# Optimization experiments

Measured on AMD Instinct MI355X. Metric: run time of the kernel, lower is better.

Reference implementation:

```python
import jax, jax.numpy as jnp
import numpy as np

B, T_IN, H, V, MAXLEN = 128, 256, 512, 32, 128


def gru_cell(x, h, Wih, Whh, bih, bhh):
    # torch GRU cell: gates ordered (r, z, n)
    gi = x @ Wih.T + bih            # [B, 3H]
    gh = h @ Whh.T + bhh            # [B, 3H]
    ir, iz, inn = jnp.split(gi, 3, axis=-1)
    hr, hz, hn = jnp.split(gh, 3, axis=-1)
    r = jax.nn.sigmoid(ir + hr)
    z = jax.nn.sigmoid(iz + hz)
    n = jnp.tanh(inn + r * hn)
    return (1.0 - z) * n + z * h


def run_gru_layer(xs, Wih, Whh, bih, bhh):
    # xs: [B, T, D] -> outputs [B, T, H], final hidden [B, H]
    h0 = jnp.zeros((xs.shape[0], Whh.shape[1]), xs.dtype)

    def step(h, x):
        hn = gru_cell(x, h, Wih, Whh, bih, bhh)
        return hn, hn

    hT, ys = jax.lax.scan(step, h0, jnp.swapaxes(xs, 0, 1))
    return jnp.swapaxes(ys, 0, 1), hT


def setup_inputs() -> dict:
    key = jax.random.key(0)
    ks = jax.random.split(key, 24)
    s = 1.0 / np.sqrt(H)

    def p(k, shape):
        return (jax.random.normal(k, shape, jnp.float32) * s).astype(jnp.float32)

    return {
        "x": jax.random.normal(ks[0], (B, T_IN, 2), jnp.float32),
        "emb": p(ks[1], (V, H)),
        # encoder GRU: layer0 input dim 2, layer1 input dim H
        "enc_Wih0": p(ks[2], (3 * H, 2)), "enc_Whh0": p(ks[3], (3 * H, H)),
        "enc_bih0": p(ks[4], (3 * H,)), "enc_bhh0": p(ks[5], (3 * H,)),
        "enc_Wih1": p(ks[6], (3 * H, H)), "enc_Whh1": p(ks[7], (3 * H, H)),
        "enc_bih1": p(ks[8], (3 * H,)), "enc_bhh1": p(ks[9], (3 * H,)),
        # decoder GRU: layer0 input dim 2H (embedded+context), layer1 input dim H
        "dec_Wih0": p(ks[10], (3 * H, 2 * H)), "dec_Whh0": p(ks[11], (3 * H, H)),
        "dec_bih0": p(ks[12], (3 * H,)), "dec_bhh0": p(ks[13], (3 * H,)),
        "dec_Wih1": p(ks[14], (3 * H, H)), "dec_Whh1": p(ks[15], (3 * H, H)),
        "dec_bih1": p(ks[16], (3 * H,)), "dec_bhh1": p(ks[17], (3 * H,)),
        "q_W": p(ks[18], (H, H)), "q_b": p(ks[19], (H,)),
        "out_W": p(ks[20], (V, H)), "out_b": p(ks[21], (V,)),
    }


def reference(x, emb,
              enc_Wih0, enc_Whh0, enc_bih0, enc_bhh0,
              enc_Wih1, enc_Whh1, enc_bih1, enc_bhh1,
              dec_Wih0, dec_Whh0, dec_bih0, dec_bhh0,
              dec_Wih1, dec_Whh1, dec_bih1, dec_bhh1,
              q_W, q_b, out_W, out_b):
    # ----- encoder: 2-layer GRU over trajectory points -----
    y0, h0 = run_gru_layer(x, enc_Wih0, enc_Whh0, enc_bih0, enc_bhh0)
    enc_outs, h1 = run_gru_layer(y0, enc_Wih1, enc_Whh1, enc_bih1, enc_bhh1)
    hidden0 = jnp.stack([h0, h1])                      # [L, B, H]
    bsz = x.shape[0]

    def step(carry, _):
        hidden, tok = carry                            # [L,B,H], [B] int
        embedded = emb[tok]                            # [B, H]
        query = hidden[-1] @ q_W.T + q_b               # [B, H]
        scores = jnp.einsum('bh,bth->bt', query, enc_outs)
        attn_w = jax.nn.softmax(scores, axis=-1)       # [B, T_in]
        context = jnp.einsum('bt,bth->bh', attn_w, enc_outs)
        rnn_in = jnp.concatenate([embedded, context], axis=-1)  # [B, 2H]
        g0 = gru_cell(rnn_in, hidden[0], dec_Wih0, dec_Whh0, dec_bih0, dec_bhh0)
        g1 = gru_cell(g0, hidden[1], dec_Wih1, dec_Whh1, dec_bih1, dec_bhh1)
        logits = g1 @ out_W.T + out_b                  # [B, V]
        tok_next = jnp.argmax(logits, axis=-1)
        return (jnp.stack([g0, g1]), tok_next), (logits, attn_w)

    tok0 = jnp.zeros((bsz,), jnp.int32)
    (hidden_f, _), (logits_seq, attn_seq) = jax.lax.scan(
        step, (hidden0, tok0), None, length=MAXLEN)
    vec_out = jnp.swapaxes(logits_seq, 0, 1)           # [B, max_len, V]
    attn = jnp.swapaxes(attn_seq, 0, 1)                # [B, max_len, T_in]
    return vec_out, hidden_f, attn
```

## Files before the change

kernel.cpp:

```cpp
#include <hip/hip_runtime.h>
#include <math.h>

#define BB 128
#define TT 256
#define HH 512
#define VV 32
#define MLEN 128
#define SLOT 65536

#define WT_OFF 0
#define QT_OFF 24576
#define PR_OFF 26624
#define SC_OFF 28416
#define SM_FLOATS 32512

typedef long long ll;

struct P {
    const float *x, *emb;
    const float *eWih0, *eWhh0, *ebih0, *ebhh0;
    const float *eWih1, *eWhh1, *ebih1, *ebhh1;
    const float *dWih0, *dWhh0, *dbih0, *dbhh0;
    const float *dWih1, *dWhh1, *dbih1, *dbhh1;
    const float *qW, *qb, *outW, *outb;
    float *ws;
    float *vecO, *hidO, *attnO;
};

__device__ __forceinline__ float sigf(float v) { return 1.0f / (1.0f + __expf(-v)); }

__device__ __forceinline__ float ldA(const float* p) {
    return __hip_atomic_load(p, __ATOMIC_RELAXED, __HIP_MEMORY_SCOPE_AGENT);
}
__device__ __forceinline__ void stA(float* p, float v) {
    __hip_atomic_store(p, v, __ATOMIC_RELAXED, __HIP_MEMORY_SCOPE_AGENT);
}
__device__ __forceinline__ int ldAi(const int* p) {
    return __hip_atomic_load(p, __ATOMIC_RELAXED, __HIP_MEMORY_SCOPE_AGENT);
}
__device__ __forceinline__ void stAi(int* p, int v) {
    __hip_atomic_store(p, v, __ATOMIC_RELAXED, __HIP_MEMORY_SCOPE_AGENT);
}

__device__ __forceinline__ void gbar(int* W, int target) {
    __syncthreads();
    if (threadIdx.x == 0) {
        int par = target & 1;
        int g = blockIdx.x & 15;
        int* gc = W + 32 + (par * 16 + g) * 32;
        if (__hip_atomic_fetch_add(gc, 1, __ATOMIC_RELAXED, __HIP_MEMORY_SCOPE_AGENT) == 15) {
            __hip_atomic_store(gc, 0, __ATOMIC_RELAXED, __HIP_MEMORY_SCOPE_AGENT);
            int* rc = W + 1056 + par * 32;
            if (__hip_atomic_fetch_add(rc, 1, __ATOMIC_RELAXED, __HIP_MEMORY_SCOPE_AGENT) == 15) {
                __hip_atomic_store(rc, 0, __ATOMIC_RELAXED, __HIP_MEMORY_SCOPE_AGENT);
                __hip_atomic_store(W, target, __ATOMIC_RELAXED, __HIP_MEMORY_SCOPE_AGENT);
            }
        }
        while (__hip_atomic_load(W, __ATOMIC_RELAXED, __HIP_MEMORY_SCOPE_AGENT) < target)
            __builtin_amdgcn_s_sleep(2);
    }
    __syncthreads();
}

__global__ __launch_bounds__(512, 1) void kmain(P p) {
    __shared__ __align__(16) float smu[SM_FLOATS];
    const int tid = threadIdx.x;
    const int lane = tid & 63;
    const int wv = tid >> 6;
    const int blk = blockIdx.x;

    int* W = (int*)p.ws;
    int* tok = W + 4096;
    float* f = (float*)p.ws + 8192;
    float* eh0 = f;
    float* eh1 = f + 2 * SLOT;
    float* inp = f + 4 * SLOT;
    float* qbm = f + 5 * SLOT;
    float* scoresB = f + 6 * SLOT;
    float* T = f + 6 * SLOT + SLOT / 2;
    float* xT = T + 3 * HH * VV;
    float* encO = f + (SLOT / 4) * 33;

    const float4* t4 = (const float4*)smu;
    const float4* t4q = (const float4*)(smu + QT_OFF);

    const int jg = blk >> 1;
    const int bh = blk & 1;
    const int b2 = bh * 64 + lane;
    int bar = 0;

    {
        stA(eh0 + blk * 1024 + tid, 0.0f);
        stA(eh0 + blk * 1024 + 512 + tid, 0.0f);
        if (tid < 256) {
            int idx = blk * 256 + tid;
            int t = idx >> 8, c = (idx >> 7) & 1, b = idx & 127;
            stA(xT + idx, p.x[((ll)b * TT + t) * 2 + c]);
        }
        if (tid < 192) {
            int unit = blk * 192 + tid;
            int v = unit & 31, gj = unit >> 5;
            const float* wrow = p.dWih0 + (ll)gj * 1024;
            const float* erow = p.emb + (ll)v * HH;
            float acc = 0.0f;
#pragma unroll 8
            for (int d = 0; d < HH; ++d) acc = fmaf(wrow[d], erow[d], acc);
            stA(T + unit, acc);
        }
#pragma unroll
        for (int jl = 0; jl < 4; ++jl)
            smu[QT_OFF + jl * 512 + tid] = p.qW[((ll)(jg * 4 + jl)) * HH + tid];
#pragma unroll
        for (int r = 0; r < 24; ++r) {
            int g = r >> 2, jl = r & 3, j = jg * 4 + jl;
            const float* src = (g < 3) ? (p.eWhh0 + (ll)(g * HH + j) * HH)
                                       : (p.eWih1 + (ll)((g - 3) * HH + j) * HH);
            smu[WT_OFF + r * 512 + tid] = src[tid];
        }
#pragma unroll
        for (int r = 0; r < 12; ++r) {
            int g = r >> 2, jl = r & 3, j = jg * 4 + jl;
            smu[WT_OFF + (24 + r) * 512 + tid] = p.eWhh1[(ll)(g * HH + j) * HH + tid];
        }
        gbar(W, ++bar);
    }

    for (int t = 0; t <= TT; ++t) {
        const float* h0s = eh0 + (((t + 1) & 1) ? SLOT : 0);
        float*       h0d = eh0 + ((t & 1) ? SLOT : 0);
        const float* h1s = eh1 + (((t + 1) & 1) ? SLOT : 0);
        float*       h1d = eh1 + ((t & 1) ? SLOT : 0);

        smu[PR_OFF + tid] = 0.0f;
        smu[PR_OFF + 512 + tid] = 0.0f;
        smu[PR_OFF + 1024 + tid] = 0.0f;
        if (tid < 256) smu[PR_OFF + 1536 + tid] = 0.0f;
        __syncthreads();

        {
            const int ds0 = wv * 64;
            float acc[36];
#pragma unroll
            for (int r = 0; r < 36; ++r) acc[r] = 0.0f;
            float av[2][8], bv[2][8];
#pragma unroll
            for (int u = 0; u < 8; ++u) av[0][u] = ldA(h0s + (ll)(ds0 + u) * BB + b2);
#pragma unroll
            for (int u = 0; u < 8; ++u) bv[0][u] = ldA(h1s + (ll)(ds0 + u) * BB + b2);
#pragma unroll
            for (int c = 0; c < 8; ++c) {
                const int cb = c & 1, pb = cb ^ 1;
                if (c < 7) {
                    const int dn = ds0 + (c + 1) * 8;
#pragma unroll
                    for (int u = 0; u < 8; ++u) av[pb][u] = ldA(h0s + (ll)(dn + u) * BB + b2);
#pragma unroll
                    for (int u = 0; u < 8; ++u) bv[pb][u] = ldA(h1s + (ll)(dn + u) * BB + b2);
                }
                const int db = ds0 + c * 8;
#pragma unroll
                for (int h2 = 0; h2 < 2; ++h2) {
                    const int q4 = (db + h2 * 4) >> 2;
#pragma unroll
                    for (int r = 0; r < 24; ++r) {
                        float4 w = t4[r * 128 + q4];
                        acc[r] = fmaf(w.x, av[cb][h2 * 4 + 0], acc[r]);
                        acc[r] = fmaf(w.y, av[cb][h2 * 4 + 1], acc[r]);
                        acc[r] = fmaf(w.z, av[cb][h2 * 4 + 2], acc[r]);
                        acc[r] = fmaf(w.w, av[cb][h2 * 4 + 3], acc[r]);
                    }
#pragma unroll
                    for (int r = 0; r < 12; ++r) {
                        float4 w = t4[(24 + r) * 128 + q4];
                        acc[24 + r] = fmaf(w.x, bv[cb][h2 * 4 + 0], acc[24 + r]);
                        acc[24 + r] = fmaf(w.y, bv[cb][h2 * 4 + 1], acc[24 + r]);
                        acc[24 + r] = fmaf(w.z, bv[cb][h2 * 4 + 2], acc[24 + r]);
                        acc[24 + r] = fmaf(w.w, bv[cb][h2 * 4 + 3], acc[24 + r]);
                    }
                }
            }
#pragma unroll
            for (int r = 0; r < 24; ++r)
                unsafeAtomicAdd(&smu[PR_OFF + r * 64 + lane], acc[r]);
#pragma unroll
            for (int r = 0; r < 12; ++r) {
                int g = r >> 2;
                int prow = (g < 2) ? (12 + g * 4) : 24;
                unsafeAtomicAdd(&smu[PR_OFF + (prow + (r & 3)) * 64 + lane], acc[24 + r]);
            }
        }
        __syncthreads();

        if (wv < 4) {
            if (t < TT) {
                int jl = wv, j = jg * 4 + jl;
                float* pr = smu + PR_OFF;
                float hr = pr[(0 + jl) * 64 + lane] + p.ebhh0[j];
                float hz = pr[(4 + jl) * 64 + lane] + p.ebhh0[HH + j];
                float hn = pr[(8 + jl) * 64 + lane] + p.ebhh0[2 * HH + j];
                float x0 = xT[t * 256 + b2], x1 = xT[t * 256 + 128 + b2];
                float ir = fmaf(p.eWih0[j * 2], x0, fmaf(p.eWih0[j * 2 + 1], x1, p.ebih0[j]));
                float iz = fmaf(p.eWih0[(HH + j) * 2], x0, fmaf(p.eWih0[(HH + j) * 2 + 1], x1, p.ebih0[HH + j]));
                float in_ = fmaf(p.eWih0[(2 * HH + j) * 2], x0, fmaf(p.eWih0[(2 * HH + j) * 2 + 1], x1, p.ebih0[2 * HH + j]));
                float r = sigf(ir + hr), z = sigf(iz + hz);
                float n = tanhf(in_ + r * hn);
                float hp = ldA(h0s + (ll)j * BB + b2);
                stA(h0d + (ll)j * BB + b2, (1.0f - z) * n + z * hp);
            }
        } else if (t >= 1) {
            int jl = wv - 4, j = jg * 4 + jl;
            float* pr = smu + PR_OFF;
            float rs = pr[(12 + jl) * 64 + lane] + p.ebih1[j] + p.ebhh1[j];
            float zs = pr[(16 + jl) * 64 + lane] + p.ebih1[HH + j] + p.ebhh1[HH + j];
            float in1 = pr[(20 + jl) * 64 + lane] + p.ebih1[2 * HH + j];
            float hn1 = pr[(24 + jl) * 64 + lane] + p.ebhh1[2 * HH + j];
            float r = sigf(rs), z = sigf(zs);
            float n = tanhf(in1 + r * hn1);
            float hp = ldA(h1s + (ll)j * BB + b2);
            float hv = (1.0f - z) * n + z * hp;
            stA(h1d + (ll)j * BB + b2, hv);
            stA(encO + ((ll)(t - 1) * HH + j) * BB + b2, hv);
        }
        gbar(W, ++bar);
    }

    {
        const float* h1c = eh1;
        if (tid < 256) smu[PR_OFF + tid] = 0.0f;
#pragma unroll
        for (int r = 0; r < 12; ++r) {
            int g = r >> 2, jl = r & 3, j = jg * 4 + jl;
            smu[WT_OFF + r * 1024 + tid]              = p.dWih0[(ll)(g * HH + j) * 1024 + 512 + tid];
            smu[WT_OFF + r * 1024 + 512 + tid]        = p.dWhh0[(ll)(g * HH + j) * HH + tid];
            smu[WT_OFF + (12 + r) * 1024 + tid]       = p.dWih1[(ll)(g * HH + j) * HH + tid];
            smu[WT_OFF + (12 + r) * 1024 + 512 + tid] = p.dWhh1[(ll)(g * HH + j) * HH + tid];
        }
        __syncthreads();
        {
            const int ds0 = wv * 64;
            float acc[4] = {0, 0, 0, 0};
            float av[8];
            for (int c = 0; c < 8; ++c) {
                int db = ds0 + c * 8;
#pragma unroll
                for (int u = 0; u < 8; ++u) av[u] = ldA(h1c + (ll)(db + u) * BB + b2);
#pragma unroll
                for (int h2 = 0; h2 < 2; ++h2) {
                    int q4 = (db + h2 * 4) >> 2;
#pragma unroll
                    for (int jl = 0; jl < 4; ++jl) {
                        float4 w = t4q[jl * 128 + q4];
                        acc[jl] = fmaf(w.x, av[h2 * 4 + 0], acc[jl]);
                        acc[jl] = fmaf(w.y, av[h2 * 4 + 1], acc[jl]);
                        acc[jl] = fmaf(w.z, av[h2 * 4 + 2], acc[jl]);
                        acc[jl] = fmaf(w.w, av[h2 * 4 + 3], acc[jl]);
                    }
                }
            }
#pragma unroll
            for (int jl = 0; jl < 4; ++jl)
                unsafeAtomicAdd(&smu[PR_OFF + jl * 64 + lane], acc[jl]);
        }
        __syncthreads();
        if (wv < 4) {
            int j = jg * 4 + wv;
            stA(qbm + (ll)j * BB + b2, smu[PR_OFF + wv * 64 + lane] + p.qb[j]);
        }
        if (blk == 128 && tid < BB) stAi(tok + tid, 0);
        gbar(W, ++bar);
    }

    for (int s = 0; s < MLEN; ++s) {
        const float* h0s = eh0 + (((s + 1) & 1) ? SLOT : 0);
        float*       g0d = eh0 + ((s & 1) ? SLOT : 0);
        const float* h1s = eh1 + ((s & 1) ? SLOT : 0);
        float*       h1d = eh1 + (((s + 1) & 1) ? SLOT : 0);

        {
            const int t0 = (blk >> 1) * 2;
            if (tid < 128) smu[PR_OFF + tid] = 0.0f;
            __syncthreads();
            const int js = wv * 64;
            float a0 = 0.0f, a1 = 0.0f;
            float qv[2][8], e0[2][8], e1[2][8];
#pragma unroll
            for (int u = 0; u < 8; ++u) {
                qv[0][u] = ldA(qbm + (ll)(js + u) * BB + b2);
                e0[0][u] = encO[((ll)t0 * HH + js + u) * BB + b2];
                e1[0][u] = encO[((ll)(t0 + 1) * HH + js + u) * BB + b2];
            }
#pragma unroll
            for (int c = 0; c < 8; ++c) {
                const int cb = c & 1, pb = cb ^ 1;
                if (c < 7) {
                    const int jn = js + (c + 1) * 8;
#pragma unroll
                    for (int u = 0; u < 8; ++u) {
                        qv[pb][u] = ldA(qbm + (ll)(jn + u) * BB + b2);
                        e0[pb][u] = encO[((ll)t0 * HH + jn + u) * BB + b2];
                        e1[pb][u] = encO[((ll)(t0 + 1) * HH + jn + u) * BB + b2];
                    }
                }
#pragma unroll
                for (int u = 0; u < 8; ++u) {
                    a0 = fmaf(qv[cb][u], e0[cb][u], a0);
                    a1 = fmaf(qv[cb][u], e1[cb][u], a1);
                }
            }
            unsafeAtomicAdd(&smu[PR_OFF + lane], a0);
            unsafeAtomicAdd(&smu[PR_OFF + 64 + lane], a1);
            __syncthreads();
            if (wv < 2)
                stA(scoresB + (ll)(t0 + wv) * BB + b2, smu[PR_OFF + wv * 64 + lane]);
        }
        gbar(W, ++bar);

        {
            const int d0 = jg * 4;
            float sv[32];
#pragma unroll
            for (int k = 0; k < 32; ++k) sv[k] = ldA(scoresB + (ll)(wv * 32 + k) * BB + b2);
            if (tid < 256) smu[PR_OFF + tid] = 0.0f;
            float mp = sv[0];
#pragma unroll
            for (int k = 1; k < 32; ++k) mp = fmaxf(mp, sv[k]);
            smu[SC_OFF + wv * 64 + lane] = mp;
            __syncthreads();
            float m = smu[SC_OFF + lane];
#pragma unroll
            for (int u = 1; u < 8; ++u) m = fmaxf(m, smu[SC_OFF + u * 64 + lane]);
            float e[32], lp = 0.0f;
#pragma unroll
            for (int k = 0; k < 32; ++k) { e[k] = __expf(sv[k] - m); lp += e[k]; }
            smu[SC_OFF + 512 + wv * 64 + lane] = lp;
            __syncthreads();
            float l = smu[SC_OFF + 512 + lane];
#pragma unroll
            for (int u = 1; u < 8; ++u) l += smu[SC_OFF + 512 + u * 64 + lane];
            float rl = 1.0f / l;
            if (blk < 16 && wv == jg) {
#pragma unroll
                for (int k = 0; k < 32; ++k) smu[SC_OFF + 1024 + k * 65 + lane] = e[k] * rl;
            }
            float c4[4] = {0, 0, 0, 0};
            float ev[2][32];
#pragma unroll
            for (int u = 0; u < 8; ++u) {
                const float* Ep = encO + ((ll)(wv * 32 + u) * HH + d0) * BB + b2;
#pragma unroll
                for (int q = 0; q < 4; ++q) ev[0][u * 4 + q] = Ep[q * BB];
            }
#pragma unroll
            for (int kb = 0; kb < 4; ++kb) {
                const int cb = kb & 1, pb = cb ^ 1;
                if (kb < 3) {
#pragma unroll
                    for (int u = 0; u < 8; ++u) {
                        const float* Ep = encO + ((ll)(wv * 32 + (kb + 1) * 8 + u) * HH + d0) * BB + b2;
#pragma unroll
                        for (int q = 0; q < 4; ++q) ev[pb][u * 4 + q] = Ep[q * BB];
                    }
                }
#pragma unroll
                for (int u = 0; u < 8; ++u) {
                    const int k = kb * 8 + u;
                    c4[0] = fmaf(e[k], ev[cb][u * 4 + 0], c4[0]);
                    c4[1] = fmaf(e[k], ev[cb][u * 4 + 1], c4[1]);
                    c4[2] = fmaf(e[k], ev[cb][u * 4 + 2], c4[2]);
                    c4[3] = fmaf(e[k], ev[cb][u * 4 + 3], c4[3]);
                }
            }
#pragma unroll
            for (int kk = 0; kk < 4; ++kk)
                unsafeAtomicAdd(&smu[PR_OFF + kk * 64 + lane], c4[kk]);
            __syncthreads();
            if (tid < 256) {
                int kk = tid >> 6, ln = tid & 63;
                float l2 = smu[SC_OFF + 512 + ln];
#pragma unroll
                for (int u = 1; u < 8; ++u) l2 += smu[SC_OFF + 512 + u * 64 + ln];
                float val = smu[PR_OFF + kk * 64 + ln] / l2;
                stA(inp + (ll)(d0 + kk) * BB + bh * 64 + ln, val);
            }
            if (blk < 16) {
                int bi = tid >> 3, tj = tid & 7;
#pragma unroll
                for (int u = 0; u < 4; ++u) {
                    int tl = tj * 4 + u;
                    p.attnO[((ll)(bh * 64 + bi) * MLEN + s) * TT + jg * 32 + tl] = smu[SC_OFF + 1024 + tl * 65 + bi];
                }
            }
        }
        gbar(W, ++bar);

        {
            smu[PR_OFF + tid] = 0.0f;
            smu[PR_OFF + 512 + tid] = 0.0f;
            __syncthreads();
            const int ctxw = (wv < 4);
            const float* stream = ctxw ? inp : h0s;
            const int ds0 = (wv & 3) * 128;
            const int tb = ctxw ? 0 : 512;
            float acc[12];
#pragma unroll
            for (int r = 0; r < 12; ++r) acc[r] = 0.0f;
            float av[2][8];
#pragma unroll
            for (int u = 0; u < 8; ++u) av[0][u] = ldA(stream + (ll)(ds0 + u) * BB + b2);
#pragma unroll
            for (int c = 0; c < 16; ++c) {
                const int cb = c & 1, pb = cb ^ 1;
                if (c < 15) {
                    const int dn = ds0 + (c + 1) * 8;
#pragma unroll
                    for (int u = 0; u < 8; ++u) av[pb][u] = ldA(stream + (ll)(dn + u) * BB + b2);
                }
                const int db = ds0 + c * 8;
#pragma unroll
                for (int h2 = 0; h2 < 2; ++h2) {
                    const int q4 = (tb + db + h2 * 4) >> 2;
#pragma unroll
                    for (int r = 0; r < 12; ++r) {
                        float4 w = t4[r * 256 + q4];
                        acc[r] = fmaf(w.x, av[cb][h2 * 4 + 0], acc[r]);
                        acc[r] = fmaf(w.y, av[cb][h2 * 4 + 1], acc[r]);
                        acc[r] = fmaf(w.z, av[cb][h2 * 4 + 2], acc[r]);
                        acc[r] = fmaf(w.w, av[cb][h2 * 4 + 3], acc[r]);
                    }
                }
            }
#pragma unroll
            for (int r = 0; r < 12; ++r) {
                int g = r >> 2;
                int prow = (g < 2) ? g * 4 : (ctxw ? 8 : 12);
                unsafeAtomicAdd(&smu[PR_OFF + (prow + (r & 3)) * 64 + lane], acc[r]);
            }
            __syncthreads();
            if (wv < 4) {
                int jl = wv, j = jg * 4 + jl;
                float* pr = smu + PR_OFF;
                int tokb = ldAi(tok + b2);
                float rs = T[(ll)j * 32 + tokb] + pr[(0 + jl) * 64 + lane] + p.dbih0[j] + p.dbhh0[j];
                float zs = T[(ll)(HH + j) * 32 + tokb] + pr[(4 + jl) * 64 + lane] + p.dbih0[HH + j] + p.dbhh0[HH + j];
                float ins = T[(ll)(2 * HH + j) * 32 + tokb] + pr[(8 + jl) * 64 + lane] + p.dbih0[2 * HH + j];
                float hns = pr[(12 + jl) * 64 + lane] + p.dbhh0[2 * HH + j];
                float r = sigf(rs), z = sigf(zs);
                float n = tanhf(ins + r * hns);
                float hp = ldA(h0s + (ll)j * BB + b2);
                stA(g0d + (ll)j * BB + b2, (1.0f - z) * n + z * hp);
            }
        }
        gbar(W, ++bar);

        {
            smu[PR_OFF + tid] = 0.0f;
            smu[PR_OFF + 512 + tid] = 0.0f;
            __syncthreads();
            const int iw = (wv < 4);
            const float* stream = iw ? g0d : h1s;
            const int ds0 = (wv & 3) * 128;
            const int tb = iw ? 0 : 512;
            float acc[12];
#pragma unroll
            for (int r = 0; r < 12; ++r) acc[r] = 0.0f;
            float av[2][8];
#pragma unroll
            for (int u = 0; u < 8; ++u) av[0][u] = ldA(stream + (ll)(ds0 + u) * BB + b2);
#pragma unroll
            for (int c = 0; c < 16; ++c) {
                const int cb = c & 1, pb = cb ^ 1;
                if (c < 15) {
                    const int dn = ds0 + (c + 1) * 8;
#pragma unroll
                    for (int u = 0; u < 8; ++u) av[pb][u] = ldA(stream + (ll)(dn + u) * BB + b2);
                }
                const int db = ds0 + c * 8;
#pragma unroll
                for (int h2 = 0; h2 < 2; ++h2) {
                    const int q4 = (tb + db + h2 * 4) >> 2;
#pragma unroll
                    for (int r = 0; r < 12; ++r) {
                        float4 w = t4[(12 + r) * 256 + q4];
                        acc[r] = fmaf(w.x, av[cb][h2 * 4 + 0], acc[r]);
                        acc[r] = fmaf(w.y, av[cb][h2 * 4 + 1], acc[r]);
                        acc[r] = fmaf(w.z, av[cb][h2 * 4 + 2], acc[r]);
                        acc[r] = fmaf(w.w, av[cb][h2 * 4 + 3], acc[r]);
                    }
                }
            }
#pragma unroll
            for (int r = 0; r < 12; ++r) {
                int g = r >> 2;
                int prow = (g < 2) ? g * 4 : (iw ? 8 : 12);
                unsafeAtomicAdd(&smu[PR_OFF + (prow + (r & 3)) * 64 + lane], acc[r]);
            }
            __syncthreads();
            if (wv < 4) {
                int jl = wv, j = jg * 4 + jl;
                float* pr = smu + PR_OFF;
                float rs = pr[(0 + jl) * 64 + lane] + p.dbih1[j] + p.dbhh1[j];
                float zs = pr[(4 + jl) * 64 + lane] + p.dbih1[HH + j] + p.dbhh1[HH + j];
                float ins = pr[(8 + jl) * 64 + lane] + p.dbih1[2 * HH + j];
                float hns = pr[(12 + jl) * 64 + lane] + p.dbhh1[2 * HH + j];
                float r = sigf(rs), z = sigf(zs);
                float n = tanhf(ins + r * hns);
                float hp = ldA(h1s + (ll)j * BB + b2);
                stA(h1d + (ll)j * BB + b2, (1.0f - z) * n + z * hp);
            }
        }
        gbar(W, ++bar);

        {
            const float* h1c = h1d;
            if (tid < 256) smu[PR_OFF + tid] = 0.0f;
            __syncthreads();
            {
                const int ds0 = wv * 64;
                float acc4[4] = {0, 0, 0, 0};
                float av[2][8];
#pragma unroll
                for (int u = 0; u < 8; ++u) av[0][u] = ldA(h1c + (ll)(ds0 + u) * BB + b2);
#pragma unroll
                for (int c = 0; c < 8; ++c) {
                    const int cb = c & 1, pb = cb ^ 1;
                    if (c < 7) {
                        const int dn = ds0 + (c + 1) * 8;
#pragma unroll
                        for (int u = 0; u < 8; ++u) av[pb][u] = ldA(h1c + (ll)(dn + u) * BB + b2);
                    }
                    const int db = ds0 + c * 8;
#pragma unroll
                    for (int h2 = 0; h2 < 2; ++h2) {
                        const int q4 = (db + h2 * 4) >> 2;
#pragma unroll
                        for (int jl = 0; jl < 4; ++jl) {
                            float4 w = t4q[jl * 128 + q4];
                            acc4[jl] = fmaf(w.x, av[cb][h2 * 4 + 0], acc4[jl]);
                            acc4[jl] = fmaf(w.y, av[cb][h2 * 4 + 1], acc4[jl]);
                            acc4[jl] = fmaf(w.z, av[cb][h2 * 4 + 2], acc4[jl]);
                            acc4[jl] = fmaf(w.w, av[cb][h2 * 4 + 3], acc4[jl]);
                        }
                    }
                }
#pragma unroll
                for (int jl = 0; jl < 4; ++jl)
                    unsafeAtomicAdd(&smu[PR_OFF + jl * 64 + lane], acc4[jl]);
            }
            __syncthreads();
            if (wv < 4) {
                int j = jg * 4 + wv;
                stA(qbm + (ll)j * BB + b2, smu[PR_OFF + wv * 64 + lane] + p.qb[j]);
            }
            if (blk >= 128 && blk < 160) {
                __syncthreads();
                const int bb = (blk - 128) * 4;
#pragma unroll
                for (int i = 0; i < 4; ++i) {
                    int f2 = i * 512 + tid;
                    int d = f2 >> 2, bi2 = f2 & 3;
                    smu[SC_OFF + f2] = ldA(h1c + (ll)d * BB + bb + bi2);
                }
                __syncthreads();
                if (tid < 128) {
                    const int bl = tid >> 5, v = tid & 31;
                    float acc = 0.0f;
                    for (int d4 = 0; d4 < 128; ++d4) {
                        float4 w4 = *(const float4*)(p.outW + (ll)v * HH + d4 * 4);
                        acc = fmaf(w4.x, smu[SC_OFF + (d4 * 4 + 0) * 4 + bl], acc);
                        acc = fmaf(w4.y, smu[SC_OFF + (d4 * 4 + 1) * 4 + bl], acc);
                        acc = fmaf(w4.z, smu[SC_OFF + (d4 * 4 + 2) * 4 + bl], acc);
                        acc = fmaf(w4.w, smu[SC_OFF + (d4 * 4 + 3) * 4 + bl], acc);
                    }
                    acc += p.outb[v];
                    p.vecO[((ll)(bb + bl) * MLEN + s) * VV + v] = acc;
                    smu[SC_OFF + 2048 + tid] = acc;
                }
                __syncthreads();
                if (tid < 4) {
                    int base = SC_OFF + 2048 + tid * 32;
                    float best = smu[base];
                    int bi2 = 0;
#pragma unroll
                    for (int u = 1; u < 32; ++u) {
                        float val = smu[base + u];
                        if (val > best) { best = val; bi2 = u; }
                    }
                    stAi(tok + bb + tid, bi2);
                }
            }
        }
        gbar(W, ++bar);
    }

    {
        int idx = blk * 512 + tid;
        int l = idx >> 16, rr = idx & 65535;
        int b = rr >> 9, h = rr & 511;
        const float* src = l ? eh1 : (eh0 + SLOT);
        p.hidO[idx] = ldA(src + (ll)h * BB + b);
    }
}

extern "C" void kernel_launch(void* const* d_in, const int* in_sizes, int n_in,
                              void* d_out, int out_size, void* d_ws, size_t ws_size,
                              hipStream_t stream) {
    (void)in_sizes; (void)n_in; (void)out_size; (void)ws_size;
    P prm;
    prm.x     = (const float*)d_in[0];
    prm.emb   = (const float*)d_in[1];
    prm.eWih0 = (const float*)d_in[2];
    prm.eWhh0 = (const float*)d_in[3];
    prm.ebih0 = (const float*)d_in[4];
    prm.ebhh0 = (const float*)d_in[5];
    prm.eWih1 = (const float*)d_in[6];
    prm.eWhh1 = (const float*)d_in[7];
    prm.ebih1 = (const float*)d_in[8];
    prm.ebhh1 = (const float*)d_in[9];
    prm.dWih0 = (const float*)d_in[10];
    prm.dWhh0 = (const float*)d_in[11];
    prm.dbih0 = (const float*)d_in[12];
    prm.dbhh0 = (const float*)d_in[13];
    prm.dWih1 = (const float*)d_in[14];
    prm.dWhh1 = (const float*)d_in[15];
    prm.dbih1 = (const float*)d_in[16];
    prm.dbhh1 = (const float*)d_in[17];
    prm.qW    = (const float*)d_in[18];
    prm.qb    = (const float*)d_in[19];
    prm.outW  = (const float*)d_in[20];
    prm.outb  = (const float*)d_in[21];
    prm.ws    = (float*)d_ws;
    prm.vecO  = (float*)d_out;
    prm.hidO  = prm.vecO + (ll)BB * MLEN * VV;
    prm.attnO = prm.hidO + (ll)2 * BB * HH;

    hipMemsetAsync(d_ws, 0, 16384, stream);
    void* args[] = { &prm };
    hipLaunchCooperativeKernel((void*)kmain, dim3(256), dim3(512), args, 0, stream);
}
```

Measured before the change: 29.99 ms.

## Double block size to 1024 threads and split reductions across 16 waves

Launches the cooperative kernel with 1024 threads per block instead of 512 and re-partitions every phase's reduction dimension across 16 wavefronts. Each wave now handles half as many input rows in the encoder, attention, decoder GRU, query and output matvecs. Weight staging, shared-memory zeroing, softmax partial maxima and sums, and the attention transpose are re-indexed to match. The aim is to shorten the serial per-wave dot-product chains in this latency-bound recurrence and add more waves to hide memory latency. The cost is more shared-memory atomic reduction traffic, idle waves in the gate phases, and tighter register limits at 1024 threads.

```diff
diff --git a/kernel.cpp b/kernel.cpp
--- a/kernel.cpp
+++ b/kernel.cpp
@@ -62,7 +62,7 @@
     __syncthreads();
 }
 
-__global__ __launch_bounds__(512, 1) void kmain(P p) {
+__global__ __launch_bounds__(1024, 1) void kmain(P p) {
     __shared__ __align__(16) float smu[SM_FLOATS];
     const int tid = threadIdx.x;
     const int lane = tid & 63;
@@ -91,7 +91,6 @@
 
     {
         stA(eh0 + blk * 1024 + tid, 0.0f);
-        stA(eh0 + blk * 1024 + 512 + tid, 0.0f);
         if (tid < 256) {
             int idx = blk * 256 + tid;
             int t = idx >> 8, c = (idx >> 7) & 1, b = idx & 127;
@@ -108,19 +107,27 @@
             stA(T + unit, acc);
         }
 #pragma unroll
-        for (int jl = 0; jl < 4; ++jl)
-            smu[QT_OFF + jl * 512 + tid] = p.qW[((ll)(jg * 4 + jl)) * HH + tid];
-#pragma unroll
-        for (int r = 0; r < 24; ++r) {
-            int g = r >> 2, jl = r & 3, j = jg * 4 + jl;
-            const float* src = (g < 3) ? (p.eWhh0 + (ll)(g * HH + j) * HH)
-                                       : (p.eWih1 + (ll)((g - 3) * HH + j) * HH);
-            smu[WT_OFF + r * 512 + tid] = src[tid];
-        }
-#pragma unroll
-        for (int r = 0; r < 12; ++r) {
-            int g = r >> 2, jl = r & 3, j = jg * 4 + jl;
-            smu[WT_OFF + (24 + r) * 512 + tid] = p.eWhh1[(ll)(g * HH + j) * HH + tid];
+        for (int i = 0; i < 2; ++i) {
+            int o = i * 1024 + tid;
+            smu[QT_OFF + o] = p.qW[(ll)jg * 2048 + o];
+        }
+        {
+            const int half = tid >> 9;
+            const int t5 = tid & 511;
+#pragma unroll
+            for (int r2 = 0; r2 < 12; ++r2) {
+                int r = r2 * 2 + half;
+                int g = r >> 2, jl = r & 3, j = jg * 4 + jl;
+                const float* src = (g < 3) ? (p.eWhh0 + (ll)(g * HH + j) * HH)
+                                           : (p.eWih1 + (ll)((g - 3) * HH + j) * HH);
+                smu[WT_OFF + r * 512 + t5] = src[t5];
+            }
+#pragma unroll
+            for (int r2 = 0; r2 < 6; ++r2) {
+                int r = r2 * 2 + half;
+                int g = r >> 2, jl = r & 3, j = jg * 4 + jl;
+                smu[WT_OFF + (24 + r) * 512 + t5] = p.eWhh1[(ll)(g * HH + j) * HH + t5];
+            }
         }
         gbar(W, ++bar);
     }
@@ -132,13 +139,11 @@
         float*       h1d = eh1 + ((t & 1) ? SLOT : 0);
 
         smu[PR_OFF + tid] = 0.0f;
-        smu[PR_OFF + 512 + tid] = 0.0f;
-        smu[PR_OFF + 1024 + tid] = 0.0f;
-        if (tid < 256) smu[PR_OFF + 1536 + tid] = 0.0f;
+        if (tid < 768) smu[PR_OFF + 1024 + tid] = 0.0f;
         __syncthreads();
 
         {
-            const int ds0 = wv * 64;
+            const int ds0 = wv * 32;
             float acc[36];
 #pragma unroll
             for (int r = 0; r < 36; ++r) acc[r] = 0.0f;
@@ -148,9 +153,9 @@
 #pragma unroll
             for (int u = 0; u < 8; ++u) bv[0][u] = ldA(h1s + (ll)(ds0 + u) * BB + b2);
 #pragma unroll
-            for (int c = 0; c < 8; ++c) {
+            for (int c = 0; c < 4; ++c) {
                 const int cb = c & 1, pb = cb ^ 1;
-                if (c < 7) {
+                if (c < 3) {
                     const int dn = ds0 + (c + 1) * 8;
 #pragma unroll
                     for (int u = 0; u < 8; ++u) av[pb][u] = ldA(h0s + (ll)(dn + u) * BB + b2);
@@ -207,19 +212,21 @@
                 float hp = ldA(h0s + (ll)j * BB + b2);
                 stA(h0d + (ll)j * BB + b2, (1.0f - z) * n + z * hp);
             }
-        } else if (t >= 1) {
-            int jl = wv - 4, j = jg * 4 + jl;
-            float* pr = smu + PR_OFF;
-            float rs = pr[(12 + jl) * 64 + lane] + p.ebih1[j] + p.ebhh1[j];
-            float zs = pr[(16 + jl) * 64 + lane] + p.ebih1[HH + j] + p.ebhh1[HH + j];
-            float in1 = pr[(20 + jl) * 64 + lane] + p.ebih1[2 * HH + j];
-            float hn1 = pr[(24 + jl) * 64 + lane] + p.ebhh1[2 * HH + j];
-            float r = sigf(rs), z = sigf(zs);
-            float n = tanhf(in1 + r * hn1);
-            float hp = ldA(h1s + (ll)j * BB + b2);
-            float hv = (1.0f - z) * n + z * hp;
-            stA(h1d + (ll)j * BB + b2, hv);
-            stA(encO + ((ll)(t - 1) * HH + j) * BB + b2, hv);
+        } else if (wv < 8) {
+            if (t >= 1) {
+                int jl = wv - 4, j = jg * 4 + jl;
+                float* pr = smu + PR_OFF;
+                float rs = pr[(12 + jl) * 64 + lane] + p.ebih1[j] + p.ebhh1[j];
+                float zs = pr[(16 + jl) * 64 + lane] + p.ebih1[HH + j] + p.ebhh1[HH + j];
+                float in1 = pr[(20 + jl) * 64 + lane] + p.ebih1[2 * HH + j];
+                float hn1 = pr[(24 + jl) * 64 + lane] + p.ebhh1[2 * HH + j];
+                float r = sigf(rs), z = sigf(zs);
+                float n = tanhf(in1 + r * hn1);
+                float hp = ldA(h1s + (ll)j * BB + b2);
+                float hv = (1.0f - z) * n + z * hp;
+                stA(h1d + (ll)j * BB + b2, hv);
+                stA(encO + ((ll)(t - 1) * HH + j) * BB + b2, hv);
+            }
         }
         gbar(W, ++bar);
     }
@@ -230,17 +237,20 @@
 #pragma unroll
         for (int r = 0; r < 12; ++r) {
             int g = r >> 2, jl = r & 3, j = jg * 4 + jl;
-            smu[WT_OFF + r * 1024 + tid]              = p.dWih0[(ll)(g * HH + j) * 1024 + 512 + tid];
-            smu[WT_OFF + r * 1024 + 512 + tid]        = p.dWhh0[(ll)(g * HH + j) * HH + tid];
-            smu[WT_OFF + (12 + r) * 1024 + tid]       = p.dWih1[(ll)(g * HH + j) * HH + tid];
-            smu[WT_OFF + (12 + r) * 1024 + 512 + tid] = p.dWhh1[(ll)(g * HH + j) * HH + tid];
+            if (tid < 512) {
+                smu[WT_OFF + r * 1024 + tid]        = p.dWih0[(ll)(g * HH + j) * 1024 + 512 + tid];
+                smu[WT_OFF + (12 + r) * 1024 + tid] = p.dWih1[(ll)(g * HH + j) * HH + tid];
+            } else {
+                smu[WT_OFF + r * 1024 + tid]        = p.dWhh0[(ll)(g * HH + j) * HH + (tid - 512)];
+                smu[WT_OFF + (12 + r) * 1024 + tid] = p.dWhh1[(ll)(g * HH + j) * HH + (tid - 512)];
+            }
         }
         __syncthreads();
         {
-            const int ds0 = wv * 64;
+            const int ds0 = wv * 32;
             float acc[4] = {0, 0, 0, 0};
             float av[8];
-            for (int c = 0; c < 8; ++c) {
+            for (int c = 0; c < 4; ++c) {
                 int db = ds0 + c * 8;
 #pragma unroll
                 for (int u = 0; u < 8; ++u) av[u] = ldA(h1c + (ll)(db + u) * BB + b2);
@@ -280,7 +290,7 @@
             const int t0 = (blk >> 1) * 2;
             if (tid < 128) smu[PR_OFF + tid] = 0.0f;
             __syncthreads();
-            const int js = wv * 64;
+            const int js = wv * 32;
             float a0 = 0.0f, a1 = 0.0f;
             float qv[2][8], e0[2][8], e1[2][8];
 #pragma unroll
@@ -290,9 +300,9 @@
                 e1[0][u] = encO[((ll)(t0 + 1) * HH + js + u) * BB + b2];
             }
 #pragma unroll
-            for (int c = 0; c < 8; ++c) {
+            for (int c = 0; c < 4; ++c) {
                 const int cb = c & 1, pb = cb ^ 1;
-                if (c < 7) {
+                if (c < 3) {
                     const int jn = js + (c + 1) * 8;
 #pragma unroll
                     for (int u = 0; u < 8; ++u) {
@@ -317,36 +327,37 @@
 
         {
             const int d0 = jg * 4;
-            float sv[32];
-#pragma unroll
-            for (int k = 0; k < 32; ++k) sv[k] = ldA(scoresB + (ll)(wv * 32 + k) * BB + b2);
+            float sv[16];
+#pragma unroll
+            for (int k = 0; k < 16; ++k) sv[k] = ldA(scoresB + (ll)(wv * 16 + k) * BB + b2);
             if (tid < 256) smu[PR_OFF + tid] = 0.0f;
             float mp = sv[0];
 #pragma unroll
-            for (int k = 1; k < 32; ++k) mp = fmaxf(mp, sv[k]);
+            for (int k = 1; k < 16; ++k) mp = fmaxf(mp, sv[k]);
             smu[SC_OFF + wv * 64 + lane] = mp;
             __syncthreads();
             float m = smu[SC_OFF + lane];
 #pragma unroll
-            for (int u = 1; u < 8; ++u) m = fmaxf(m, smu[SC_OFF + u * 64 + lane]);
-            float e[32], lp = 0.0f;
-#pragma unroll
-            for (int k = 0; k < 32; ++k) { e[k] = __expf(sv[k] - m); lp += e[k]; }
-            smu[SC_OFF + 512 + wv * 64 + lane] = lp;
-            __syncthreads();
-            float l = smu[SC_OFF + 512 + lane];
-#pragma unroll
-            for (int u = 1; u < 8; ++u) l += smu[SC_OFF + 512 + u * 64 + lane];
+            for (int u = 1; u < 16; ++u) m = fmaxf(m, smu[SC_OFF + u * 64 + lane]);
+            float e[16], lp = 0.0f;
+#pragma unroll
+            for (int k = 0; k < 16; ++k) { e[k] = __expf(sv[k] - m); lp += e[k]; }
+            smu[SC_OFF + 1024 + wv * 64 + lane] = lp;
+            __syncthreads();
+            float l = smu[SC_OFF + 1024 + lane];
+#pragma unroll
+            for (int u = 1; u < 16; ++u) l += smu[SC_OFF + 1024 + u * 64 + lane];
             float rl = 1.0f / l;
-            if (blk < 16 && wv == jg) {
-#pragma unroll
-                for (int k = 0; k < 32; ++k) smu[SC_OFF + 1024 + k * 65 + lane] = e[k] * rl;
+            if (blk < 16 && (wv >> 1) == jg) {
+#pragma unroll
+                for (int k = 0; k < 16; ++k)
+                    smu[SC_OFF + 2048 + ((wv & 1) * 16 + k) * 64 + lane] = e[k] * rl;
             }
             float c4[4] = {0, 0, 0, 0};
-            float ev[2][32];
-#pragma unroll
-            for (int u = 0; u < 8; ++u) {
-                const float* Ep = encO + ((ll)(wv * 32 + u) * HH + d0) * BB + b2;
+            float ev[2][16];
+#pragma unroll
+            for (int u = 0; u < 4; ++u) {
+                const float* Ep = encO + ((ll)(wv * 16 + u) * HH + d0) * BB + b2;
 #pragma unroll
                 for (int q = 0; q < 4; ++q) ev[0][u * 4 + q] = Ep[q * BB];
             }
@@ -355,15 +366,15 @@
                 const int cb = kb & 1, pb = cb ^ 1;
                 if (kb < 3) {
 #pragma unroll
-                    for (int u = 0; u < 8; ++u) {
-                        const float* Ep = encO + ((ll)(wv * 32 + (kb + 1) * 8 + u) * HH + d0) * BB + b2;
+                    for (int u = 0; u < 4; ++u) {
+                        const float* Ep = encO + ((ll)(wv * 16 + (kb + 1) * 4 + u) * HH + d0) * BB + b2;
 #pragma unroll
                         for (int q = 0; q < 4; ++q) ev[pb][u * 4 + q] = Ep[q * BB];
                     }
                 }
 #pragma unroll
-                for (int u = 0; u < 8; ++u) {
-                    const int k = kb * 8 + u;
+                for (int u = 0; u < 4; ++u) {
+                    const int k = kb * 4 + u;
                     c4[0] = fmaf(e[k], ev[cb][u * 4 + 0], c4[0]);
                     c4[1] = fmaf(e[k], ev[cb][u * 4 + 1], c4[1]);
                     c4[2] = fmaf(e[k], ev[cb][u * 4 + 2], c4[2]);
@@ -376,18 +387,19 @@
             __syncthreads();
             if (tid < 256) {
                 int kk = tid >> 6, ln = tid & 63;
-                float l2 = smu[SC_OFF + 512 + ln];
-#pragma unroll
-                for (int u = 1; u < 8; ++u) l2 += smu[SC_OFF + 512 + u * 64 + ln];
+                float l2 = smu[SC_OFF + 1024 + ln];
+#pragma unroll
+                for (int u = 1; u < 16; ++u) l2 += smu[SC_OFF + 1024 + u * 64 + ln];
                 float val = smu[PR_OFF + kk * 64 + ln] / l2;
                 stA(inp + (ll)(d0 + kk) * BB + bh * 64 + ln, val);
             }
             if (blk < 16) {
-                int bi = tid >> 3, tj = tid & 7;
-#pragma unroll
-                for (int u = 0; u < 4; ++u) {
-                    int tl = tj * 4 + u;
-                    p.attnO[((ll)(bh * 64 + bi) * MLEN + s) * TT + jg * 32 + tl] = smu[SC_OFF + 1024 + tl * 65 + bi];
+                int bi = tid >> 4, tj = tid & 15;
+#pragma unroll
+                for (int u = 0; u < 2; ++u) {
+                    int tl = tj * 2 + u;
+                    p.attnO[((ll)(bh * 64 + bi) * MLEN + s) * TT + jg * 32 + tl] =
+                        smu[SC_OFF + 2048 + tl * 64 + bi];
                 }
             }
         }
@@ -395,11 +407,10 @@
 
         {
             smu[PR_OFF + tid] = 0.0f;
-            smu[PR_OFF + 512 + tid] = 0.0f;
-            __syncthreads();
-            const int ctxw = (wv < 4);
+            __syncthreads();
+            const int ctxw = (wv < 8);
             const float* stream = ctxw ? inp : h0s;
-            const int ds0 = (wv & 3) * 128;
+            const int ds0 = (wv & 7) * 64;
             const int tb = ctxw ? 0 : 512;
             float acc[12];
 #pragma unroll
@@ -408,9 +419,9 @@
 #pragma unroll
             for (int u = 0; u < 8; ++u) av[0][u] = ldA(stream + (ll)(ds0 + u) * BB + b2);
 #pragma unroll
-            for (int c = 0; c < 16; ++c) {
+            for (int c = 0; c < 8; ++c) {
                 const int cb = c & 1, pb = cb ^ 1;
-                if (c < 15) {
+                if (c < 7) {
                     const int dn = ds0 + (c + 1) * 8;
 #pragma unroll
                     for (int u = 0; u < 8; ++u) av[pb][u] = ldA(stream + (ll)(dn + u) * BB + b2);
@@ -454,11 +465,10 @@
 
         {
             smu[PR_OFF + tid] = 0.0f;
-            smu[PR_OFF + 512 + tid] = 0.0f;
-            __syncthreads();
-            const int iw = (wv < 4);
+            __syncthreads();
+            const int iw = (wv < 8);
             const float* stream = iw ? g0d : h1s;
-            const int ds0 = (wv & 3) * 128;
+            const int ds0 = (wv & 7) * 64;
             const int tb = iw ? 0 : 512;
             float acc[12];
 #pragma unroll
@@ -467,9 +477,9 @@
 #pragma unroll
             for (int u = 0; u < 8; ++u) av[0][u] = ldA(stream + (ll)(ds0 + u) * BB + b2);
 #pragma unroll
-            for (int c = 0; c < 16; ++c) {
+            for (int c = 0; c < 8; ++c) {
                 const int cb = c & 1, pb = cb ^ 1;
-                if (c < 15) {
+                if (c < 7) {
                     const int dn = ds0 + (c + 1) * 8;
 #pragma unroll
                     for (int u = 0; u < 8; ++u) av[pb][u] = ldA(stream + (ll)(dn + u) * BB + b2);
@@ -515,15 +525,15 @@
             if (tid < 256) smu[PR_OFF + tid] = 0.0f;
             __syncthreads();
             {
-                const int ds0 = wv * 64;
+                const int ds0 = wv * 32;
                 float acc4[4] = {0, 0, 0, 0};
                 float av[2][8];
 #pragma unroll
                 for (int u = 0; u < 8; ++u) av[0][u] = ldA(h1c + (ll)(ds0 + u) * BB + b2);
 #pragma unroll
-                for (int c = 0; c < 8; ++c) {
+                for (int c = 0; c < 4; ++c) {
                     const int cb = c & 1, pb = cb ^ 1;
-                    if (c < 7) {
+                    if (c < 3) {
                         const int dn = ds0 + (c + 1) * 8;
 #pragma unroll
                         for (int u = 0; u < 8; ++u) av[pb][u] = ldA(h1c + (ll)(dn + u) * BB + b2);
@@ -555,8 +565,8 @@
                 __syncthreads();
                 const int bb = (blk - 128) * 4;
 #pragma unroll
-                for (int i = 0; i < 4; ++i) {
-                    int f2 = i * 512 + tid;
+                for (int i = 0; i < 2; ++i) {
+                    int f2 = i * 1024 + tid;
                     int d = f2 >> 2, bi2 = f2 & 3;
                     smu[SC_OFF + f2] = ldA(h1c + (ll)d * BB + bb + bi2);
                 }
@@ -592,7 +602,7 @@
         gbar(W, ++bar);
     }
 
-    {
+    if (tid < 512) {
         int idx = blk * 512 + tid;
         int l = idx >> 16, rr = idx & 65535;
         int b = rr >> 9, h = rr & 511;
@@ -635,5 +645,5 @@
 
     hipMemsetAsync(d_ws, 0, 16384, stream);
     void* args[] = { &prm };
-    hipLaunchCooperativeKernel((void*)kmain, dim3(256), dim3(512), args, 0, stream);
+    hipLaunchCooperativeKernel((void*)kmain, dim3(256), dim3(1024), args, 0, stream);
 }
```

Result: slower. 34.76 ms (+15.9%).
